# Kernel optimization log

Hardware: AMD Instinct MI355X
Metric: run time of the kernel (lower is better)

## Reference

```python
import jax, jax.numpy as jnp
import numpy as np

N = 50000    # nodes
E = 600000   # edges
H = 128      # hidden_dim
NF = 12      # n_features
L = 4        # n_layers
EPS = 1e-5   # LayerNorm eps


def setup_inputs() -> dict:
    key = jax.random.key(0)
    ks = jax.random.split(key, 32)

    def w(k, shape, fan_in):
        return (jax.random.normal(k, shape, jnp.float32) / np.float32(np.sqrt(fan_in)))

    inp = {
        "x": jax.random.normal(ks[0], (N, NF), jnp.float32),
        "edge_index": jax.random.randint(ks[1], (2, E), 0, N, dtype=jnp.int64),
        # encoder: Linear(NF,H) -> ReLU -> Linear(H,H)
        "enc_W1": w(ks[2], (NF, H), NF), "enc_b1": jnp.zeros((H,), jnp.float32),
        "enc_W2": w(ks[3], (H, H), H),   "enc_b2": jnp.zeros((H,), jnp.float32),
        # L residual SAGE blocks (PyG SAGEConv: lin_l on mean-aggr w/ bias, lin_r on self no bias)
        "lin_l_W": w(ks[4], (L, H, H), H), "lin_l_b": jnp.zeros((L, H), jnp.float32),
        "lin_r_W": w(ks[5], (L, H, H), H),
        "ln_g": jnp.ones((L, H), jnp.float32), "ln_b": jnp.zeros((L, H), jnp.float32),
        # disp head: H->H->H//2->3
        "dW1": w(ks[6], (H, H), H),      "db1": jnp.zeros((H,), jnp.float32),
        "dW2": w(ks[7], (H, H // 2), H), "db2": jnp.zeros((H // 2,), jnp.float32),
        "dW3": w(ks[8], (H // 2, 3), H // 2), "db3": jnp.zeros((3,), jnp.float32),
        # stress head: H->H->H//2->1
        "sW1": w(ks[9], (H, H), H),       "sb1": jnp.zeros((H,), jnp.float32),
        "sW2": w(ks[10], (H, H // 2), H), "sb2": jnp.zeros((H // 2,), jnp.float32),
        "sW3": w(ks[11], (H // 2, 1), H // 2), "sb3": jnp.zeros((1,), jnp.float32),
    }
    return inp


def reference(x, edge_index, enc_W1, enc_b1, enc_W2, enc_b2,
              lin_l_W, lin_l_b, lin_r_W, ln_g, ln_b,
              dW1, db1, dW2, db2, dW3, db3,
              sW1, sb1, sW2, sb2, sW3, sb3):
    src, dst = edge_index[0], edge_index[1]

    # linear load-scaling ratio from load columns [3:6]
    load_mag = jnp.linalg.norm(x[:, 3:6], axis=1)
    ratio = jnp.max(load_mag)

    # encoder MLP
    h = jnp.maximum(x @ enc_W1 + enc_b1, 0.0) @ enc_W2 + enc_b2  # [N, H]

    # in-degree for mean aggregation (clamped to 1 like PyG)
    deg = jax.ops.segment_sum(jnp.ones((E,), h.dtype), dst, num_segments=N)
    inv_deg = 1.0 / jnp.clip(deg, 1.0)[:, None]  # [N, 1]

    for l in range(L):
        # SAGEConv: mean of neighbor (src) features at dst, then lin_l(aggr) + lin_r(self)
        agg = jax.ops.segment_sum(h[src], dst, num_segments=N) * inv_deg  # [N, H]
        y = agg @ lin_l_W[l] + lin_l_b[l] + h @ lin_r_W[l]
        # LayerNorm over channels
        mu = jnp.mean(y, axis=-1, keepdims=True)
        var = jnp.var(y, axis=-1, keepdims=True)
        y = (y - mu) * jax.lax.rsqrt(var + EPS) * ln_g[l] + ln_b[l]
        # residual + ReLU
        h = h + jnp.maximum(y, 0.0)

    # heads
    d = jnp.maximum(h @ dW1 + db1, 0.0)
    d = jnp.maximum(d @ dW2 + db2, 0.0) @ dW3 + db3  # [N, 3]
    s = jnp.maximum(h @ sW1 + sb1, 0.0)
    s = jnp.maximum(s @ sW2 + sb2, 0.0) @ sW3 + sb3  # [N, 1]

    # linear_scaling = True
    d = d * ratio
    s = s * ratio
    return jnp.concatenate([d, s], axis=1)  # [N, 4]
```

## Files before the change

### kernel.cpp

```cpp
#include <hip/hip_runtime.h>
#include <hip/hip_bf16.h>

typedef __hip_bfloat16 bf16;
typedef short bf16x8 __attribute__((ext_vector_type(8)));
typedef float f32x4 __attribute__((ext_vector_type(4)));

__device__ __forceinline__ float2 bfpair(unsigned u){
  float2 r; r.x = __uint_as_float(u<<16); r.y = __uint_as_float(u & 0xffff0000u); return r;
}
__device__ __forceinline__ float bfu(unsigned short u){ return __uint_as_float(((unsigned)u)<<16); }
__device__ __forceinline__ unsigned f2bf(float f){
  unsigned u = __float_as_uint(f);
  return (u + 0x7fffu + ((u>>16)&1u)) >> 16;
}
__device__ __forceinline__ unsigned fpack(float a, float b){
  return (f2bf(b)<<16) | f2bf(a);
}
__device__ __forceinline__ int edge_is64(const int* e){
  return (e[1]==0) & (e[3]==0) & (e[5]==0);
}
__device__ __forceinline__ int edge_ld(const int* e, int is64, int idx){
  return e[is64 ? 2*idx : idx];
}

__global__ void k_pre(const float* __restrict__ x, const int* __restrict__ eidx,
                      unsigned* __restrict__ ratio, int* __restrict__ deg,
                      int N, int E, int nbE){
  if((int)blockIdx.x < nbE){
    int e = blockIdx.x*blockDim.x + threadIdx.x;
    if(e>=E) return;
    int is64 = edge_is64(eidx);
    int d = edge_ld(eidx, is64, E+e);
    if((unsigned)d < (unsigned)N) atomicAdd(&deg[d], 1);
  } else {
    int i = (blockIdx.x-nbE)*blockDim.x + threadIdx.x;
    int stride = 256*blockDim.x;
    float m = 0.f;
    for(; i<N; i+=stride){
      float a = x[(size_t)i*12+3];
      float b = x[(size_t)i*12+4];
      float c = x[(size_t)i*12+5];
      m = fmaxf(m, sqrtf(a*a+b*b+c*c));
    }
    #pragma unroll
    for(int off=1; off<64; off<<=1) m = fmaxf(m, __shfl_xor(m, off));
    if((threadIdx.x & 63)==0) atomicMax(ratio, __float_as_uint(m));
  }
}

__global__ void k_scan1(const int* __restrict__ deg, int* __restrict__ bsum, int N){
  int t = threadIdx.x;
  int idx0 = blockIdx.x*1024 + t*4;
  int s=0;
  #pragma unroll
  for(int i=0;i<4;i++){ int idx=idx0+i; if(idx<N) s += deg[idx]; }
  #pragma unroll
  for(int off=1; off<64; off<<=1) s += __shfl_xor(s, off);
  __shared__ int ws4[4];
  if((t&63)==0) ws4[t>>6]=s;
  __syncthreads();
  if(t==0) bsum[blockIdx.x]=ws4[0]+ws4[1]+ws4[2]+ws4[3];
}
__global__ void k_scan2w(int* bsum, int nb){
  int lane = threadIdx.x;
  if(nb <= 64){
    int v = (lane<nb)? bsum[lane] : 0;
    int incl = v;
    #pragma unroll
    for(int off=1; off<64; off<<=1){ int t = __shfl_up(incl, (unsigned)off); if(lane>=off) incl+=t; }
    if(lane<nb) bsum[lane] = incl - v;
  } else if(lane==0){
    int acc=0;
    for(int i=0;i<nb;i++){ int v=bsum[i]; bsum[i]=acc; acc+=v; }
  }
}
__global__ void k_scan3(const int* __restrict__ deg, const int* __restrict__ bsum,
                        int* __restrict__ offs, int* __restrict__ pos,
                        float* __restrict__ invdeg, int N, int E){
  int t = threadIdx.x;
  int idx0 = blockIdx.x*1024 + t*4;
  int d[4]; int s=0;
  #pragma unroll
  for(int i=0;i<4;i++){ int idx=idx0+i; d[i] = (idx<N)? deg[idx]:0; s+=d[i]; }
  int lane=t&63, w=t>>6;
  int incl=s;
  #pragma unroll
  for(int off=1; off<64; off<<=1){ int v=__shfl_up(incl, (unsigned)off); if(lane>=off) incl+=v; }
  __shared__ int wsum[4];
  if(lane==63) wsum[w]=incl;
  __syncthreads();
  int base = bsum[blockIdx.x];
  for(int i=0;i<w;i++) base += wsum[i];
  int run = base + incl - s;
  #pragma unroll
  for(int i=0;i<4;i++){
    int idx=idx0+i;
    if(idx<N){
      offs[idx]=run; pos[idx]=run;
      invdeg[idx] = 1.0f / (float)(d[i]>0? d[i]:1);
    }
    run += d[i];
  }
  if(blockIdx.x==0 && t==0) offs[N]=E;
}

__global__ void k_bucket(const int* __restrict__ eidx, int* __restrict__ pos,
                         int* __restrict__ csr, int E, int N){
  int e = blockIdx.x*blockDim.x + threadIdx.x;
  if(e>=E) return;
  int is64 = edge_is64(eidx);
  int d = edge_ld(eidx, is64, E+e);
  int s = edge_ld(eidx, is64, e);
  if((unsigned)d >= (unsigned)N) return;
  if((unsigned)s >= (unsigned)N) s = 0;
  int p = atomicAdd(&pos[d], 1);
  if((unsigned)p < (unsigned)E) csr[p] = s;
}

__global__ void k_wconv_all(
    const float* __restrict__ llW, const float* __restrict__ lrW,
    const float* __restrict__ dW1, const float* __restrict__ sW1,
    const float* __restrict__ dW2, const float* __restrict__ sW2,
    const float* __restrict__ eW2,
    unsigned short* __restrict__ WTs, unsigned short* __restrict__ WT1,
    unsigned short* __restrict__ WT2, unsigned short* __restrict__ WE2){
  int idx = blockIdx.x*256 + threadIdx.x;
  int j = idx & 7;
  int lane = (idx>>3) & 63;
  int q = lane >> 4, p = lane & 15;
  if(idx < 131072){
    int nt = (idx>>9) & 7, ks = (idx>>12) & 7, l = (idx>>15) & 3;
    int k = ks*32 + q*8 + j, n = nt*16 + p;
    float v = (k<128) ? llW[(size_t)l*16384 + (size_t)k*128 + n]
                      : lrW[(size_t)l*16384 + (size_t)(k-128)*128 + n];
    WTs[idx] = (unsigned short)f2bf(v);
  } else if(idx < 163840){
    int i2 = idx - 131072;
    int nt = (i2>>9) & 15, ks = (i2>>13) & 3;
    int k = ks*32 + q*8 + j, n = nt*16 + p;
    float v = (n<128) ? dW1[(size_t)k*128 + n] : sW1[(size_t)k*128 + (n-128)];
    WT1[i2] = (unsigned short)f2bf(v);
  } else if(idx < 180224){
    int i2 = idx - 163840;
    int nt = (i2>>9) & 7, ks = (i2>>12) & 3;
    int k = ks*32 + q*8 + j, n = nt*16 + p;
    float v = (n<64) ? dW2[(size_t)k*64 + n] : sW2[(size_t)k*64 + (n-64)];
    WT2[i2] = (unsigned short)f2bf(v);
  } else if(idx < 196608){
    int i2 = idx - 180224;
    int nt = (i2>>9) & 7, ks = (i2>>12) & 3;
    int k = ks*32 + q*8 + j, n = nt*16 + p;
    WE2[i2] = (unsigned short)f2bf(eW2[(size_t)k*128 + n]);
  }
}

__global__ __launch_bounds__(256) void k_aggregate(
    const bf16* __restrict__ h, bf16* __restrict__ agg,
    const int* __restrict__ offs, const int* __restrict__ csr,
    const float* __restrict__ invdeg, int N, int E){
  int row = blockIdx.x*8 + (threadIdx.x>>5);
  int l = threadIdx.x & 31;
  if(row >= N) return;
  int s = offs[row], e = offs[row+1];
  s = max(0, min(s, E)); e = max(s, min(e, E));
  float a0=0.f, a1=0.f, a2=0.f, a3=0.f;
  int i = s;
  for(; i+4<=e; i+=4){
    int j0=csr[i], j1=csr[i+1], j2=csr[i+2], j3=csr[i+3];
    uint2 u0 = *(const uint2*)(h + (size_t)j0*128 + l*4);
    uint2 u1 = *(const uint2*)(h + (size_t)j1*128 + l*4);
    uint2 u2 = *(const uint2*)(h + (size_t)j2*128 + l*4);
    uint2 u3 = *(const uint2*)(h + (size_t)j3*128 + l*4);
    float2 p0=bfpair(u0.x), q0=bfpair(u0.y);
    float2 p1=bfpair(u1.x), q1=bfpair(u1.y);
    float2 p2=bfpair(u2.x), q2=bfpair(u2.y);
    float2 p3=bfpair(u3.x), q3=bfpair(u3.y);
    a0 += p0.x+p1.x+p2.x+p3.x;
    a1 += p0.y+p1.y+p2.y+p3.y;
    a2 += q0.x+q1.x+q2.x+q3.x;
    a3 += q0.y+q1.y+q2.y+q3.y;
  }
  for(; i<e; ++i){
    int j = csr[i];
    uint2 u = *(const uint2*)(h + (size_t)j*128 + l*4);
    float2 p=bfpair(u.x), q=bfpair(u.y);
    a0+=p.x; a1+=p.y; a2+=q.x; a3+=q.y;
  }
  float id = invdeg[row];
  uint2 o; o.x = fpack(a0*id, a1*id); o.y = fpack(a2*id, a3*id);
  *(uint2*)(agg + (size_t)row*128 + l*4) = o;
}

__global__ __launch_bounds__(256) void k_encoder(
  const float* __restrict__ x,
  const float* __restrict__ W1, const float* __restrict__ b1,
  const unsigned short* __restrict__ WE2, const float* __restrict__ b2,
  bf16* __restrict__ h, int N)
{
  __shared__ float Xs[64][12];
  __shared__ float W1s[12][128];
  __shared__ float b1s[128];
  __shared__ __align__(16) unsigned short T1b[64][136];
  int tid = threadIdx.x;
  int tx = tid & 31, ty = tid >> 5;
  int rowBase = blockIdx.x*64;
  for(int idx=tid; idx<768; idx+=256){
    int r = idx/12, c = idx - r*12;
    int row = rowBase + r;
    Xs[r][c] = (row<N)? x[(size_t)row*12+c] : 0.f;
  }
  for(int idx=tid; idx<1536; idx+=256) W1s[idx>>7][idx&127] = W1[idx];
  if(tid<128) b1s[tid] = b1[tid];
  __syncthreads();
  float acc[8][4] = {};
  #pragma unroll
  for(int k=0;k<12;k++){
    float4 w4 = *(float4*)&W1s[k][tx*4];
    #pragma unroll
    for(int r=0;r<8;r++){
      float a = Xs[ty*8+r][k];
      acc[r][0]+=a*w4.x; acc[r][1]+=a*w4.y; acc[r][2]+=a*w4.z; acc[r][3]+=a*w4.w;
    }
  }
  #pragma unroll
  for(int r=0;r<8;r++)
    #pragma unroll
    for(int c=0;c<4;c++)
      T1b[ty*8+r][tx*4+c] = (unsigned short)f2bf(fmaxf(acc[r][c] + b1s[tx*4+c], 0.f));
  __syncthreads();

  int lane = tid & 63;
  int w = tid >> 6, q = lane >> 4, p = lane & 15;
  f32x4 acc2[8];
  #pragma unroll
  for(int nt=0; nt<8; nt++) acc2[nt] = (f32x4){0.f,0.f,0.f,0.f};
  #pragma unroll
  for(int ks=0; ks<4; ks++){
    bf16x8 af = *(const bf16x8*)&T1b[w*16+p][ks*32+q*8];
    #pragma unroll
    for(int nt=0; nt<8; nt++){
      bf16x8 bfr = *(const bf16x8*)(WE2 + ((size_t)(ks*8+nt)*64 + lane)*8);
      acc2[nt] = __builtin_amdgcn_mfma_f32_16x16x32_bf16(af, bfr, acc2[nt], 0,0,0);
    }
  }
  float b2v[8];
  #pragma unroll
  for(int nt=0; nt<8; nt++) b2v[nt] = b2[nt*16+p];
  unsigned short* hu = (unsigned short*)h;
  #pragma unroll
  for(int r=0;r<4;r++){
    int row = rowBase + w*16 + q*4 + r;
    if(row < N){
      #pragma unroll
      for(int nt=0; nt<8; nt++)
        hu[(size_t)row*128 + nt*16+p] = (unsigned short)f2bf(acc2[nt][r] + b2v[nt]);
    }
  }
}

__global__ __launch_bounds__(256) void k_sage_mfma(
    bf16* __restrict__ h, const bf16* __restrict__ agg,
    const unsigned short* __restrict__ WT,
    const float* __restrict__ bl, const float* __restrict__ lng,
    const float* __restrict__ lnb, int N)
{
  int tid = threadIdx.x;
  int lane = tid & 63;
  int w = tid >> 6;
  int q = lane >> 4;
  int p = lane & 15;
  int rowBase = blockIdx.x*64;

  int am = rowBase + w*16 + p;
  bool arow_ok = am < N;
  const unsigned short* aggRow = (const unsigned short*)agg + (size_t)am*128;
  const unsigned short* hRow   = (const unsigned short*)h   + (size_t)am*128;

  f32x4 acc[8];
  #pragma unroll
  for(int nt=0; nt<8; nt++) acc[nt] = (f32x4){0.f,0.f,0.f,0.f};

  #pragma unroll
  for(int ks=0; ks<8; ks++){
    int koff = ks*32 + q*8;
    bf16x8 afrag = {0,0,0,0,0,0,0,0};
    if(arow_ok){
      const unsigned short* src = (koff < 128) ? (aggRow + koff) : (hRow + (koff-128));
      afrag = *(const bf16x8*)src;
    }
    #pragma unroll
    for(int nt=0; nt<8; nt++){
      bf16x8 bfrag = *(const bf16x8*)(WT + ((size_t)(ks*8+nt)*64 + lane)*8);
      acc[nt] = __builtin_amdgcn_mfma_f32_16x16x32_bf16(afrag, bfrag, acc[nt], 0, 0, 0);
    }
  }

  float blv[8], gvv[8], bvv[8];
  #pragma unroll
  for(int nt=0; nt<8; nt++){
    int col = nt*16 + p;
    blv[nt] = bl[col]; gvv[nt] = lng[col]; bvv[nt] = lnb[col];
  }
  unsigned short* hu = (unsigned short*)h;
  #pragma unroll
  for(int r=0; r<4; r++){
    int row = rowBase + w*16 + q*4 + r;
    float y[8]; float s = 0.f, sq = 0.f;
    #pragma unroll
    for(int nt=0; nt<8; nt++){
      float v = acc[nt][r] + blv[nt];
      y[nt] = v; s += v; sq += v*v;
    }
    #pragma unroll
    for(int off=1; off<16; off<<=1){ s += __shfl_xor(s, off); sq += __shfl_xor(sq, off); }
    float mu = s*(1.f/128.f);
    float var = fmaxf(sq*(1.f/128.f) - mu*mu, 0.f);
    float rstd = rsqrtf(var + 1e-5f);
    if(row < N){
      #pragma unroll
      for(int nt=0; nt<8; nt++){
        int col = nt*16 + p;
        float hv = bfu(hu[(size_t)row*128 + col]);
        float o = hv + fmaxf((y[nt]-mu)*rstd*gvv[nt] + bvv[nt], 0.f);
        hu[(size_t)row*128 + col] = (unsigned short)f2bf(o);
      }
    }
  }
}

__global__ __launch_bounds__(256) void k_heads_mfma(
  const bf16* __restrict__ h,
  const unsigned short* __restrict__ WT1,
  const unsigned short* __restrict__ WT2,
  const float* __restrict__ db1, const float* __restrict__ sb1,
  const float* __restrict__ db2, const float* __restrict__ sb2,
  const float* __restrict__ dW3, const float* __restrict__ db3,
  const float* __restrict__ sW3, const float* __restrict__ sb3,
  const float* __restrict__ ratio_p, float* __restrict__ out, int N)
{
  __shared__ __align__(16) unsigned short T1s[4][16][264];
  const float ratio = *ratio_p;
  int tid = threadIdx.x;
  int lane = tid & 63;
  int w = tid >> 6;
  int q = lane >> 4;
  int p = lane & 15;
  int rowBase = blockIdx.x*64;
  int am = rowBase + w*16 + p;
  bool arow_ok = am < N;
  const unsigned short* hRow = (const unsigned short*)h + (size_t)am*128;

  f32x4 acc1[16];
  #pragma unroll
  for(int nt=0; nt<16; nt++) acc1[nt] = (f32x4){0.f,0.f,0.f,0.f};
  #pragma unroll
  for(int ks=0; ks<4; ks++){
    int koff = ks*32 + q*8;
    bf16x8 af = {0,0,0,0,0,0,0,0};
    if(arow_ok) af = *(const bf16x8*)(hRow + koff);
    #pragma unroll
    for(int nt=0; nt<16; nt++){
      bf16x8 bfr = *(const bf16x8*)(WT1 + ((size_t)(ks*16+nt)*64 + lane)*8);
      acc1[nt] = __builtin_amdgcn_mfma_f32_16x16x32_bf16(af, bfr, acc1[nt], 0,0,0);
    }
  }
  #pragma unroll
  for(int nt=0; nt<16; nt++){
    float b1v = (nt<8) ? db1[nt*16+p] : sb1[(nt-8)*16+p];
    #pragma unroll
    for(int r=0;r<4;r++){
      float v = fmaxf(acc1[nt][r] + b1v, 0.f);
      T1s[w][q*4+r][nt*16+p] = (unsigned short)f2bf(v);
    }
  }
  __syncthreads();

  f32x4 acc2[8];
  #pragma unroll
  for(int nt=0; nt<8; nt++) acc2[nt] = (f32x4){0.f,0.f,0.f,0.f};
  #pragma unroll
  for(int ks=0; ks<4; ks++){
    int koff = ks*32 + q*8;
    bf16x8 ad = *(const bf16x8*)&T1s[w][p][koff];
    bf16x8 as = *(const bf16x8*)&T1s[w][p][128+koff];
    #pragma unroll
    for(int nt=0; nt<8; nt++){
      bf16x8 bfr = *(const bf16x8*)(WT2 + ((size_t)(ks*8+nt)*64 + lane)*8);
      acc2[nt] = __builtin_amdgcn_mfma_f32_16x16x32_bf16(nt<4? ad : as, bfr, acc2[nt], 0,0,0);
    }
  }

  float w3d[4][3], w3s[4], bd2[4], bs2[4];
  #pragma unroll
  for(int nt=0; nt<4; nt++){
    #pragma unroll
    for(int c=0;c<3;c++) w3d[nt][c] = dW3[(nt*16+p)*3 + c];
    w3s[nt] = sW3[nt*16+p];
    bd2[nt] = db2[nt*16+p];
    bs2[nt] = sb2[nt*16+p];
  }
  float b3v = (p==0)? db3[0] : (p==1)? db3[1] : (p==2)? db3[2] : sb3[0];
  #pragma unroll
  for(int r=0;r<4;r++){
    int row = rowBase + w*16 + q*4 + r;
    float pd0=0.f, pd1=0.f, pd2=0.f, ps=0.f;
    #pragma unroll
    for(int nt=0; nt<4; nt++){
      float td = fmaxf(acc2[nt][r]   + bd2[nt], 0.f);
      float ts = fmaxf(acc2[nt+4][r] + bs2[nt], 0.f);
      pd0 += td*w3d[nt][0]; pd1 += td*w3d[nt][1]; pd2 += td*w3d[nt][2];
      ps  += ts*w3s[nt];
    }
    #pragma unroll
    for(int off=1; off<16; off<<=1){
      pd0 += __shfl_xor(pd0, off); pd1 += __shfl_xor(pd1, off);
      pd2 += __shfl_xor(pd2, off); ps  += __shfl_xor(ps, off);
    }
    if(row < N && p < 4){
      float v = (p==0)? pd0 : (p==1)? pd1 : (p==2)? pd2 : ps;
      out[(size_t)row*4 + p] = (v + b3v)*ratio;
    }
  }
}

extern "C" void kernel_launch(void* const* d_in, const int* in_sizes, int n_in,
                              void* d_out, int out_size, void* d_ws, size_t ws_size,
                              hipStream_t stream)
{
  const float* x   = (const float*)d_in[0];
  const int*  eidx = (const int*) d_in[1];
  const float* eW1 = (const float*)d_in[2];
  const float* eb1 = (const float*)d_in[3];
  const float* eW2 = (const float*)d_in[4];
  const float* eb2 = (const float*)d_in[5];
  const float* llW = (const float*)d_in[6];
  const float* llb = (const float*)d_in[7];
  const float* lrW = (const float*)d_in[8];
  const float* lng = (const float*)d_in[9];
  const float* lnb = (const float*)d_in[10];
  const float* dW1 = (const float*)d_in[11];
  const float* db1 = (const float*)d_in[12];
  const float* dW2 = (const float*)d_in[13];
  const float* db2 = (const float*)d_in[14];
  const float* dW3 = (const float*)d_in[15];
  const float* db3 = (const float*)d_in[16];
  const float* sW1 = (const float*)d_in[17];
  const float* sb1 = (const float*)d_in[18];
  const float* sW2 = (const float*)d_in[19];
  const float* sb2 = (const float*)d_in[20];
  const float* sW3 = (const float*)d_in[21];
  const float* sb3 = (const float*)d_in[22];
  float* out = (float*)d_out;

  const int N = in_sizes[0] / 12;
  const int E = in_sizes[1] / 2;
  (void)n_in; (void)out_size; (void)ws_size;

  char* base = (char*)d_ws;
  size_t off = 0;
  auto alloc = [&](size_t nbytes)->char*{
    char* p = base + off; off += (nbytes + 255) & ~(size_t)255; return p;
  };
  unsigned* ratio = (unsigned*)alloc(4);
  int*   deg    = (int*)  alloc((size_t)N*4);
  int*   offs   = (int*)  alloc(((size_t)N+1)*4);
  int*   pos    = (int*)  alloc((size_t)N*4);
  int*   bsum   = (int*)  alloc(256*4);
  int*   csr    = (int*)  alloc((size_t)E*4);
  float* invdeg = (float*)alloc((size_t)N*4);
  bf16*  hA     = (bf16*) alloc((size_t)N*128*2);
  bf16*  agg    = (bf16*) alloc((size_t)N*128*2);
  unsigned short* WTs  = (unsigned short*)alloc((size_t)131072*2);
  unsigned short* WT1h = (unsigned short*)alloc((size_t)32768*2);
  unsigned short* WT2h = (unsigned short*)alloc((size_t)16384*2);
  unsigned short* WE2  = (unsigned short*)alloc((size_t)16384*2);

  size_t zbytes = (size_t)((char*)offs - base);
  hipMemsetAsync(d_ws, 0, zbytes, stream);

  int nbE    = (E + 255)/256;
  int nbScan = (N + 1023)/1024;
  int nbTile = (N + 63)/64;
  int nbAgg  = (N + 7)/8;

  k_pre   <<<nbE + 256, 256, 0, stream>>>(x, eidx, ratio, deg, N, E, nbE);
  k_scan1 <<<nbScan, 256, 0, stream>>>(deg, bsum, N);
  k_scan2w<<<1, 64, 0, stream>>>(bsum, nbScan);
  k_scan3 <<<nbScan, 256, 0, stream>>>(deg, bsum, offs, pos, invdeg, N, E);
  k_bucket<<<nbE, 256, 0, stream>>>(eidx, pos, csr, E, N);
  k_wconv_all<<<768, 256, 0, stream>>>(llW, lrW, dW1, sW1, dW2, sW2, eW2,
                                       WTs, WT1h, WT2h, WE2);

  k_encoder<<<nbTile, 256, 0, stream>>>(x, eW1, eb1, WE2, eb2, hA, N);
  for(int l=0;l<4;l++){
    k_aggregate<<<nbAgg, 256, 0, stream>>>(hA, agg, offs, csr, invdeg, N, E);
    k_sage_mfma<<<nbTile, 256, 0, stream>>>(hA, agg,
        WTs + (size_t)l*32768,
        llb + (size_t)l*128, lng + (size_t)l*128, lnb + (size_t)l*128, N);
  }
  k_heads_mfma<<<nbTile, 256, 0, stream>>>(hA, WT1h, WT2h,
      db1, sb1, db2, sb2, dW3, db3, sW3, sb3, (const float*)ratio, out, N);
}
```

Baseline: 390.4 us.

## Fuse neighbor aggregation into SAGE MFMA kernel via shared memory

Merges the separate aggregation kernel into the per-layer MFMA kernel: each 64-row block first gathers and averages neighbor features into an LDS tile, then runs the GEMM reading the aggregated half from LDS. Hidden state now ping-pongs between two buffers because other blocks still read the previous layer's h. This removes the agg buffer's global write and read plus one launch per layer. In exchange, each block does gather work then GEMM serially with fewer blocks (64 rows per block vs 8), which may reduce latency hiding for the irregular gather.

```diff
diff --git a/kernel.cpp b/kernel.cpp
--- a/kernel.cpp
+++ b/kernel.cpp
@@ -154,43 +154,6 @@
   }
 }
 
-__global__ __launch_bounds__(256) void k_aggregate(
-    const bf16* __restrict__ h, bf16* __restrict__ agg,
-    const int* __restrict__ offs, const int* __restrict__ csr,
-    const float* __restrict__ invdeg, int N, int E){
-  int row = blockIdx.x*8 + (threadIdx.x>>5);
-  int l = threadIdx.x & 31;
-  if(row >= N) return;
-  int s = offs[row], e = offs[row+1];
-  s = max(0, min(s, E)); e = max(s, min(e, E));
-  float a0=0.f, a1=0.f, a2=0.f, a3=0.f;
-  int i = s;
-  for(; i+4<=e; i+=4){
-    int j0=csr[i], j1=csr[i+1], j2=csr[i+2], j3=csr[i+3];
-    uint2 u0 = *(const uint2*)(h + (size_t)j0*128 + l*4);
-    uint2 u1 = *(const uint2*)(h + (size_t)j1*128 + l*4);
-    uint2 u2 = *(const uint2*)(h + (size_t)j2*128 + l*4);
-    uint2 u3 = *(const uint2*)(h + (size_t)j3*128 + l*4);
-    float2 p0=bfpair(u0.x), q0=bfpair(u0.y);
-    float2 p1=bfpair(u1.x), q1=bfpair(u1.y);
-    float2 p2=bfpair(u2.x), q2=bfpair(u2.y);
-    float2 p3=bfpair(u3.x), q3=bfpair(u3.y);
-    a0 += p0.x+p1.x+p2.x+p3.x;
-    a1 += p0.y+p1.y+p2.y+p3.y;
-    a2 += q0.x+q1.x+q2.x+q3.x;
-    a3 += q0.y+q1.y+q2.y+q3.y;
-  }
-  for(; i<e; ++i){
-    int j = csr[i];
-    uint2 u = *(const uint2*)(h + (size_t)j*128 + l*4);
-    float2 p=bfpair(u.x), q=bfpair(u.y);
-    a0+=p.x; a1+=p.y; a2+=q.x; a3+=q.y;
-  }
-  float id = invdeg[row];
-  uint2 o; o.x = fpack(a0*id, a1*id); o.y = fpack(a2*id, a3*id);
-  *(uint2*)(agg + (size_t)row*128 + l*4) = o;
-}
-
 __global__ __launch_bounds__(256) void k_encoder(
   const float* __restrict__ x,
   const float* __restrict__ W1, const float* __restrict__ b1,
@@ -258,23 +221,67 @@
   }
 }
 
-__global__ __launch_bounds__(256) void k_sage_mfma(
-    bf16* __restrict__ h, const bf16* __restrict__ agg,
+__global__ __launch_bounds__(256) void k_layer(
+    const bf16* __restrict__ hin, bf16* __restrict__ hout,
+    const int* __restrict__ offs, const int* __restrict__ csr,
+    const float* __restrict__ invdeg,
     const unsigned short* __restrict__ WT,
     const float* __restrict__ bl, const float* __restrict__ lng,
-    const float* __restrict__ lnb, int N)
+    const float* __restrict__ lnb, int N, int E)
 {
+  __shared__ __align__(16) unsigned short Ag[64][136];
   int tid = threadIdx.x;
+  int rowBase = blockIdx.x*64;
+
+  {
+    int hw = tid >> 5;
+    int l  = tid & 31;
+    #pragma unroll
+    for(int i=0;i<8;i++){
+      int r = hw*8 + i;
+      int row = rowBase + r;
+      float a0=0.f, a1=0.f, a2=0.f, a3=0.f;
+      if(row < N){
+        int s = offs[row], e = offs[row+1];
+        s = max(0, min(s, E)); e = max(s, min(e, E));
+        int it = s;
+        for(; it+4<=e; it+=4){
+          int j0=csr[it], j1=csr[it+1], j2=csr[it+2], j3=csr[it+3];
+          uint2 u0 = *(const uint2*)(hin + (size_t)j0*128 + l*4);
+          uint2 u1 = *(const uint2*)(hin + (size_t)j1*128 + l*4);
+          uint2 u2 = *(const uint2*)(hin + (size_t)j2*128 + l*4);
+          uint2 u3 = *(const uint2*)(hin + (size_t)j3*128 + l*4);
+          float2 p0=bfpair(u0.x), q0=bfpair(u0.y);
+          float2 p1=bfpair(u1.x), q1=bfpair(u1.y);
+          float2 p2=bfpair(u2.x), q2=bfpair(u2.y);
+          float2 p3=bfpair(u3.x), q3=bfpair(u3.y);
+          a0 += p0.x+p1.x+p2.x+p3.x;
+          a1 += p0.y+p1.y+p2.y+p3.y;
+          a2 += q0.x+q1.x+q2.x+q3.x;
+          a3 += q0.y+q1.y+q2.y+q3.y;
+        }
+        for(; it<e; ++it){
+          int j = csr[it];
+          uint2 u = *(const uint2*)(hin + (size_t)j*128 + l*4);
+          float2 pp=bfpair(u.x), qq=bfpair(u.y);
+          a0+=pp.x; a1+=pp.y; a2+=qq.x; a3+=qq.y;
+        }
+        float id = invdeg[row];
+        a0*=id; a1*=id; a2*=id; a3*=id;
+      }
+      uint2 o; o.x = fpack(a0,a1); o.y = fpack(a2,a3);
+      *(uint2*)&Ag[r][l*4] = o;
+    }
+  }
+  __syncthreads();
+
   int lane = tid & 63;
   int w = tid >> 6;
   int q = lane >> 4;
   int p = lane & 15;
-  int rowBase = blockIdx.x*64;
-
   int am = rowBase + w*16 + p;
   bool arow_ok = am < N;
-  const unsigned short* aggRow = (const unsigned short*)agg + (size_t)am*128;
-  const unsigned short* hRow   = (const unsigned short*)h   + (size_t)am*128;
+  const unsigned short* hRow = (const unsigned short*)hin + (size_t)am*128;
 
   f32x4 acc[8];
   #pragma unroll
@@ -282,11 +289,12 @@
 
   #pragma unroll
   for(int ks=0; ks<8; ks++){
-    int koff = ks*32 + q*8;
-    bf16x8 afrag = {0,0,0,0,0,0,0,0};
-    if(arow_ok){
-      const unsigned short* src = (koff < 128) ? (aggRow + koff) : (hRow + (koff-128));
-      afrag = *(const bf16x8*)src;
+    bf16x8 afrag;
+    if(ks < 4){
+      afrag = *(const bf16x8*)&Ag[w*16+p][ks*32 + q*8];
+    } else {
+      afrag = (bf16x8){0,0,0,0,0,0,0,0};
+      if(arow_ok) afrag = *(const bf16x8*)(hRow + (ks-4)*32 + q*8);
     }
     #pragma unroll
     for(int nt=0; nt<8; nt++){
@@ -301,7 +309,8 @@
     int col = nt*16 + p;
     blv[nt] = bl[col]; gvv[nt] = lng[col]; bvv[nt] = lnb[col];
   }
-  unsigned short* hu = (unsigned short*)h;
+  const unsigned short* hiu = (const unsigned short*)hin;
+  unsigned short* hou = (unsigned short*)hout;
   #pragma unroll
   for(int r=0; r<4; r++){
     int row = rowBase + w*16 + q*4 + r;
@@ -320,9 +329,9 @@
       #pragma unroll
       for(int nt=0; nt<8; nt++){
         int col = nt*16 + p;
-        float hv = bfu(hu[(size_t)row*128 + col]);
+        float hv = bfu(hiu[(size_t)row*128 + col]);
         float o = hv + fmaxf((y[nt]-mu)*rstd*gvv[nt] + bvv[nt], 0.f);
-        hu[(size_t)row*128 + col] = (unsigned short)f2bf(o);
+        hou[(size_t)row*128 + col] = (unsigned short)f2bf(o);
       }
     }
   }
@@ -469,7 +478,7 @@
   int*   csr    = (int*)  alloc((size_t)E*4);
   float* invdeg = (float*)alloc((size_t)N*4);
   bf16*  hA     = (bf16*) alloc((size_t)N*128*2);
-  bf16*  agg    = (bf16*) alloc((size_t)N*128*2);
+  bf16*  hB     = (bf16*) alloc((size_t)N*128*2);
   unsigned short* WTs  = (unsigned short*)alloc((size_t)131072*2);
   unsigned short* WT1h = (unsigned short*)alloc((size_t)32768*2);
   unsigned short* WT2h = (unsigned short*)alloc((size_t)16384*2);
@@ -481,7 +490,6 @@
   int nbE    = (E + 255)/256;
   int nbScan = (N + 1023)/1024;
   int nbTile = (N + 63)/64;
-  int nbAgg  = (N + 7)/8;
 
   k_pre   <<<nbE + 256, 256, 0, stream>>>(x, eidx, ratio, deg, N, E, nbE);
   k_scan1 <<<nbScan, 256, 0, stream>>>(deg, bsum, N);
@@ -492,12 +500,13 @@
                                        WTs, WT1h, WT2h, WE2);
 
   k_encoder<<<nbTile, 256, 0, stream>>>(x, eW1, eb1, WE2, eb2, hA, N);
+  bf16* hin = hA; bf16* hout = hB;
   for(int l=0;l<4;l++){
-    k_aggregate<<<nbAgg, 256, 0, stream>>>(hA, agg, offs, csr, invdeg, N, E);
-    k_sage_mfma<<<nbTile, 256, 0, stream>>>(hA, agg,
+    k_layer<<<nbTile, 256, 0, stream>>>(hin, hout, offs, csr, invdeg,
         WTs + (size_t)l*32768,
-        llb + (size_t)l*128, lng + (size_t)l*128, lnb + (size_t)l*128, N);
-  }
-  k_heads_mfma<<<nbTile, 256, 0, stream>>>(hA, WT1h, WT2h,
+        llb + (size_t)l*128, lng + (size_t)l*128, lnb + (size_t)l*128, N, E);
+    bf16* t = hin; hin = hout; hout = t;
+  }
+  k_heads_mfma<<<nbTile, 256, 0, stream>>>(hin, WT1h, WT2h,
       db1, sb1, db2, sb2, dW3, db3, sW3, sb3, (const float*)ratio, out, N);
 }
```

After: 530.5 us. 35.9% more time.

## Fuse scan and bucket/weight-convert kernels; widen aggregate gather to 16-byte loads

Applied to the files above, without the earlier changes.

Folds the single-block block-sum scan into every k_scan3 block, which now rescans the up to 64 block sums in shared memory. It also merges the edge bucketing and weight conversion into one launch, cutting the setup stage from six launches to four. The aggregation kernel now uses 16 lanes per row with 16-byte bf16 loads, so each wave covers 4 rows instead of 2. The fused scan assumes nbScan is at most 64, which holds for N=50000 but drops the old serial fallback for larger N.

```diff
diff --git a/kernel.cpp b/kernel.cpp
--- a/kernel.cpp
+++ b/kernel.cpp
@@ -61,23 +61,19 @@
   __syncthreads();
   if(t==0) bsum[blockIdx.x]=ws4[0]+ws4[1]+ws4[2]+ws4[3];
 }
-__global__ void k_scan2w(int* bsum, int nb){
-  int lane = threadIdx.x;
-  if(nb <= 64){
-    int v = (lane<nb)? bsum[lane] : 0;
-    int incl = v;
-    #pragma unroll
-    for(int off=1; off<64; off<<=1){ int t = __shfl_up(incl, (unsigned)off); if(lane>=off) incl+=t; }
-    if(lane<nb) bsum[lane] = incl - v;
-  } else if(lane==0){
-    int acc=0;
-    for(int i=0;i<nb;i++){ int v=bsum[i]; bsum[i]=acc; acc+=v; }
-  }
-}
 __global__ void k_scan3(const int* __restrict__ deg, const int* __restrict__ bsum,
                         int* __restrict__ offs, int* __restrict__ pos,
-                        float* __restrict__ invdeg, int N, int E){
+                        float* __restrict__ invdeg, int N, int E, int nb){
+  __shared__ int sb[64];
   int t = threadIdx.x;
+  if(t < 64){
+    int v = (t<nb)? bsum[t] : 0;
+    int incl = v;
+    #pragma unroll
+    for(int off=1; off<64; off<<=1){ int u = __shfl_up(incl, (unsigned)off); if(t>=off) incl+=u; }
+    sb[t] = incl - v;
+  }
+  __syncthreads();
   int idx0 = blockIdx.x*1024 + t*4;
   int d[4]; int s=0;
   #pragma unroll
@@ -89,7 +85,7 @@
   __shared__ int wsum[4];
   if(lane==63) wsum[w]=incl;
   __syncthreads();
-  int base = bsum[blockIdx.x];
+  int base = sb[blockIdx.x];
   for(int i=0;i<w;i++) base += wsum[i];
   int run = base + incl - s;
   #pragma unroll
@@ -104,27 +100,28 @@
   if(blockIdx.x==0 && t==0) offs[N]=E;
 }
 
-__global__ void k_bucket(const int* __restrict__ eidx, int* __restrict__ pos,
-                         int* __restrict__ csr, int E, int N){
-  int e = blockIdx.x*blockDim.x + threadIdx.x;
-  if(e>=E) return;
-  int is64 = edge_is64(eidx);
-  int d = edge_ld(eidx, is64, E+e);
-  int s = edge_ld(eidx, is64, e);
-  if((unsigned)d >= (unsigned)N) return;
-  if((unsigned)s >= (unsigned)N) s = 0;
-  int p = atomicAdd(&pos[d], 1);
-  if((unsigned)p < (unsigned)E) csr[p] = s;
-}
-
-__global__ void k_wconv_all(
+__global__ void k_bucket_wconv(
+    const int* __restrict__ eidx, int* __restrict__ pos, int* __restrict__ csr,
+    int E, int N, int nbE,
     const float* __restrict__ llW, const float* __restrict__ lrW,
     const float* __restrict__ dW1, const float* __restrict__ sW1,
     const float* __restrict__ dW2, const float* __restrict__ sW2,
     const float* __restrict__ eW2,
     unsigned short* __restrict__ WTs, unsigned short* __restrict__ WT1,
     unsigned short* __restrict__ WT2, unsigned short* __restrict__ WE2){
-  int idx = blockIdx.x*256 + threadIdx.x;
+  if((int)blockIdx.x < nbE){
+    int e = blockIdx.x*256 + threadIdx.x;
+    if(e>=E) return;
+    int is64 = edge_is64(eidx);
+    int d = edge_ld(eidx, is64, E+e);
+    int s = edge_ld(eidx, is64, e);
+    if((unsigned)d >= (unsigned)N) return;
+    if((unsigned)s >= (unsigned)N) s = 0;
+    int p = atomicAdd(&pos[d], 1);
+    if((unsigned)p < (unsigned)E) csr[p] = s;
+    return;
+  }
+  int idx = (blockIdx.x - nbE)*256 + threadIdx.x;
   int j = idx & 7;
   int lane = (idx>>3) & 63;
   int q = lane >> 4, p = lane & 15;
@@ -158,37 +155,41 @@
     const bf16* __restrict__ h, bf16* __restrict__ agg,
     const int* __restrict__ offs, const int* __restrict__ csr,
     const float* __restrict__ invdeg, int N, int E){
-  int row = blockIdx.x*8 + (threadIdx.x>>5);
-  int l = threadIdx.x & 31;
+  int row = blockIdx.x*16 + (threadIdx.x>>4);
+  int l = threadIdx.x & 15;
   if(row >= N) return;
   int s = offs[row], e = offs[row+1];
   s = max(0, min(s, E)); e = max(s, min(e, E));
-  float a0=0.f, a1=0.f, a2=0.f, a3=0.f;
+  float a0=0.f,a1=0.f,a2=0.f,a3=0.f,a4=0.f,a5=0.f,a6=0.f,a7=0.f;
   int i = s;
   for(; i+4<=e; i+=4){
     int j0=csr[i], j1=csr[i+1], j2=csr[i+2], j3=csr[i+3];
-    uint2 u0 = *(const uint2*)(h + (size_t)j0*128 + l*4);
-    uint2 u1 = *(const uint2*)(h + (size_t)j1*128 + l*4);
-    uint2 u2 = *(const uint2*)(h + (size_t)j2*128 + l*4);
-    uint2 u3 = *(const uint2*)(h + (size_t)j3*128 + l*4);
-    float2 p0=bfpair(u0.x), q0=bfpair(u0.y);
-    float2 p1=bfpair(u1.x), q1=bfpair(u1.y);
-    float2 p2=bfpair(u2.x), q2=bfpair(u2.y);
-    float2 p3=bfpair(u3.x), q3=bfpair(u3.y);
-    a0 += p0.x+p1.x+p2.x+p3.x;
-    a1 += p0.y+p1.y+p2.y+p3.y;
-    a2 += q0.x+q1.x+q2.x+q3.x;
-    a3 += q0.y+q1.y+q2.y+q3.y;
+    uint4 u0 = *(const uint4*)(h + (size_t)j0*128 + l*8);
+    uint4 u1 = *(const uint4*)(h + (size_t)j1*128 + l*8);
+    uint4 u2 = *(const uint4*)(h + (size_t)j2*128 + l*8);
+    uint4 u3 = *(const uint4*)(h + (size_t)j3*128 + l*8);
+    float2 f;
+    f=bfpair(u0.x); a0+=f.x; a1+=f.y;  f=bfpair(u0.y); a2+=f.x; a3+=f.y;
+    f=bfpair(u0.z); a4+=f.x; a5+=f.y;  f=bfpair(u0.w); a6+=f.x; a7+=f.y;
+    f=bfpair(u1.x); a0+=f.x; a1+=f.y;  f=bfpair(u1.y); a2+=f.x; a3+=f.y;
+    f=bfpair(u1.z); a4+=f.x; a5+=f.y;  f=bfpair(u1.w); a6+=f.x; a7+=f.y;
+    f=bfpair(u2.x); a0+=f.x; a1+=f.y;  f=bfpair(u2.y); a2+=f.x; a3+=f.y;
+    f=bfpair(u2.z); a4+=f.x; a5+=f.y;  f=bfpair(u2.w); a6+=f.x; a7+=f.y;
+    f=bfpair(u3.x); a0+=f.x; a1+=f.y;  f=bfpair(u3.y); a2+=f.x; a3+=f.y;
+    f=bfpair(u3.z); a4+=f.x; a5+=f.y;  f=bfpair(u3.w); a6+=f.x; a7+=f.y;
   }
   for(; i<e; ++i){
-    int j = csr[i];
-    uint2 u = *(const uint2*)(h + (size_t)j*128 + l*4);
-    float2 p=bfpair(u.x), q=bfpair(u.y);
-    a0+=p.x; a1+=p.y; a2+=q.x; a3+=q.y;
+    int jj = csr[i];
+    uint4 u = *(const uint4*)(h + (size_t)jj*128 + l*8);
+    float2 f;
+    f=bfpair(u.x); a0+=f.x; a1+=f.y;  f=bfpair(u.y); a2+=f.x; a3+=f.y;
+    f=bfpair(u.z); a4+=f.x; a5+=f.y;  f=bfpair(u.w); a6+=f.x; a7+=f.y;
   }
   float id = invdeg[row];
-  uint2 o; o.x = fpack(a0*id, a1*id); o.y = fpack(a2*id, a3*id);
-  *(uint2*)(agg + (size_t)row*128 + l*4) = o;
+  uint4 o;
+  o.x = fpack(a0*id, a1*id); o.y = fpack(a2*id, a3*id);
+  o.z = fpack(a4*id, a5*id); o.w = fpack(a6*id, a7*id);
+  *(uint4*)(agg + (size_t)row*128 + l*8) = o;
 }
 
 __global__ __launch_bounds__(256) void k_encoder(
@@ -481,15 +482,13 @@
   int nbE    = (E + 255)/256;
   int nbScan = (N + 1023)/1024;
   int nbTile = (N + 63)/64;
-  int nbAgg  = (N + 7)/8;
-
-  k_pre   <<<nbE + 256, 256, 0, stream>>>(x, eidx, ratio, deg, N, E, nbE);
-  k_scan1 <<<nbScan, 256, 0, stream>>>(deg, bsum, N);
-  k_scan2w<<<1, 64, 0, stream>>>(bsum, nbScan);
-  k_scan3 <<<nbScan, 256, 0, stream>>>(deg, bsum, offs, pos, invdeg, N, E);
-  k_bucket<<<nbE, 256, 0, stream>>>(eidx, pos, csr, E, N);
-  k_wconv_all<<<768, 256, 0, stream>>>(llW, lrW, dW1, sW1, dW2, sW2, eW2,
-                                       WTs, WT1h, WT2h, WE2);
+  int nbAgg  = (N + 15)/16;
+
+  k_pre  <<<nbE + 256, 256, 0, stream>>>(x, eidx, ratio, deg, N, E, nbE);
+  k_scan1<<<nbScan, 256, 0, stream>>>(deg, bsum, N);
+  k_scan3<<<nbScan, 256, 0, stream>>>(deg, bsum, offs, pos, invdeg, N, E, nbScan);
+  k_bucket_wconv<<<nbE + 768, 256, 0, stream>>>(eidx, pos, csr, E, N, nbE,
+      llW, lrW, dW1, sW1, dW2, sW2, eW2, WTs, WT1h, WT2h, WE2);
 
   k_encoder<<<nbTile, 256, 0, stream>>>(x, eW1, eb1, WE2, eb2, hA, N);
   for(int l=0;l<4;l++){
```

Measured after the change: 376.6 us. 3.5% less time.
